# Performance work log

Measured on AMD Instinct MI355X. Metric: run time of the kernel, lower is better.

The kernel has to match this reference:

```python
import jax, jax.numpy as jnp
import numpy as np

C, PH, PW, H, W = 10, 7, 7, 34, 34
STRIDE = 8.0
S = 4  # sample_per_part


def setup_inputs() -> dict:
    key = jax.random.key(0)
    k1, k2, k3, k4, k5 = jax.random.split(key, 5)
    N = 30000
    ft = jax.random.normal(k1, (1, C * PH * PW, H, W), dtype=jnp.float32)
    x1 = jax.random.uniform(k2, (N,), dtype=jnp.float32) * 200.0
    y1 = jax.random.uniform(k3, (N,), dtype=jnp.float32) * 200.0
    bw = jax.random.uniform(k4, (N,), dtype=jnp.float32) * 70.0 + 2.0
    bh = jax.random.uniform(k5, (N,), dtype=jnp.float32) * 70.0 + 2.0
    rois = jnp.stack([jnp.zeros((N,), jnp.float32), x1, y1, x1 + bw, y1 + bh], axis=1)
    return {"ft_add_left_right": ft, "rois": rois}


def reference(ft_add_left_right, rois):
    ft = ft_add_left_right[0].reshape(C, PH, PW, H, W)
    roi_start_w = rois[:, 1] / STRIDE
    roi_start_h = rois[:, 2] / STRIDE
    roi_end_w = rois[:, 3] / STRIDE
    roi_end_h = rois[:, 4] / STRIDE
    # torch.threshold(x, 0.1, 0.1): x if x > 0.1 else 0.1
    roi_height = jnp.where(roi_end_h - roi_start_h > 0.1, roi_end_h - roi_start_h, 0.1)
    roi_width = jnp.where(roi_end_w - roi_start_w > 0.1, roi_end_w - roi_start_w, 0.1)
    bin_size_h = roi_height / PH
    bin_size_w = roi_width / PW
    sub_h = bin_size_h / S
    sub_w = bin_size_w / S

    gh, gw = jnp.meshgrid(jnp.arange(PH), jnp.arange(PW), indexing='ij')
    phs = gh.reshape(-1, 1)  # [49,1]
    pws = gw.reshape(-1, 1)  # [49,1]
    hstart = jnp.floor(roi_start_h + phs * bin_size_h)  # [49,N]
    wstart = jnp.floor(roi_start_w + pws * bin_size_w)  # [49,N]

    N = rois.shape[0]
    sum_ = jnp.zeros((C, PH * PW, N), jnp.float32)
    count = jnp.zeros((PH * PW, N), jnp.float32)

    for ih in range(S):
        for iw in range(S):
            w = wstart + (iw + 0.5) * sub_w  # [49,N]
            h = hstart + (ih + 0.5) * sub_h
            keep = (w > -1) & (w < W) & (h > -1) & (h < H)
            x1 = jnp.floor(w).astype(jnp.int32)
            x2 = jnp.ceil(w).astype(jnp.int32)
            y1 = jnp.floor(h).astype(jnp.int32)
            y2 = jnp.ceil(h).astype(jnp.int32)
            x1v = (x1 >= 0) & (x1 < W)
            x2v = (x2 >= 0) & (x2 < W)
            y1v = (y1 >= 0) & (y1 < H)
            y2v = (y2 >= 0) & (y2 < H)
            x1 = jnp.clip(x1, 0, W - 1)
            x2 = jnp.clip(x2, 0, W - 1)
            y1 = jnp.clip(y1, 0, H - 1)
            y2 = jnp.clip(y2, 0, H - 1)
            dist_x = w - x1
            dist_y = h - y1
            # gathers: result [C,49,N]
            v11 = ft[:, phs, pws, y1, x1]
            v12 = ft[:, phs, pws, y2, x1]
            v21 = ft[:, phs, pws, y1, x2]
            v22 = ft[:, phs, pws, y2, x2]
            # faithful to source: ALL four masks zero value11 only (source bug)
            bad11 = (~x1v & y1v) | (~x1v & y2v) | (~x2v & y1v) | (~x2v & y2v)
            v11 = jnp.where(bad11, 0.0, v11)
            value = ((1 - dist_x) * (1 - dist_y) * v11
                     + (1 - dist_x) * dist_y * v12
                     + dist_x * (1 - dist_y) * v21
                     + dist_x * dist_y * v22)
            sum_ = sum_ + jnp.where(keep, value, 0.0)
            count = count + keep.astype(jnp.float32)

    out = jnp.where(count > 0, sum_ / jnp.maximum(count, 1.0), sum_)
    return jnp.transpose(out, (2, 0, 1))  # [N, C, 49]
```

## Files before the change

kernel.cpp:

```cpp
#include <hip/hip_runtime.h>
#include <hip/hip_fp16.h>


#define NC 10
#define NBIN 49
#define FH 34
#define FW 34
#define PLANE (FH * FW)
#define NPIX (NBIN * PLANE)
#define RPB 16
#define TSTRIDE 491
#define NSIDE 14

__global__ __launch_bounds__(256) void prep_kernel(
    const float* __restrict__ ft, unsigned int* __restrict__ ws)
{
    const int p = blockIdx.x * 256 + threadIdx.x;
    if (p >= NPIX) return;
    unsigned int h2[5];
#pragma unroll
    for (int c = 0; c < 5; ++c) {
        const __half lo = __float2half_rn(ft[(2 * c)     * NPIX + p]);
        const __half hi = __float2half_rn(ft[(2 * c + 1) * NPIX + p]);
        const __half2 hh = __halves2half2(lo, hi);
        h2[c] = *(const unsigned int*)&hh;
    }
    *(uint4*)(ws + (size_t)p * 4) = make_uint4(h2[0], h2[1], h2[2], h2[3]);
    unsigned int* fb = ws + (size_t)NPIX * 4;
#pragma unroll
    for (int m = 0; m < 4; ++m)
        if (p >= m) fb[(size_t)m * NPIX + (p - m)] = h2[4];
}

__device__ __forceinline__ void fma2(float w, unsigned int u, float& s0, float& s1)
{
    const __half2 h = *(const __half2*)&u;
    s0 = fmaf(w, __half2float(__low2half(h)),  s0);
    s1 = fmaf(w, __half2float(__high2half(h)), s1);
}

__global__ __launch_bounds__(256) void main_kernel(
    const float* __restrict__ rois, const unsigned int* __restrict__ ftH,
    const float* __restrict__ ft, float* __restrict__ out, int N, int use_t)
{
    __shared__ float sides[NSIDE][RPB][8];
    __shared__ float tile[RPB][TSTRIDE];

    const int r = threadIdx.x & (RPB - 1);
    const int s = threadIdx.x >> 4;
    const int n = blockIdx.x * RPB + r;
    const bool valid = (n < N);

    float rsw = 0.f, rsh = 0.f, rew = 0.f, reh = 0.f;
    if (valid) {
        rsw = rois[n * 5 + 1] * 0.125f;
        rsh = rois[n * 5 + 2] * 0.125f;
        rew = rois[n * 5 + 3] * 0.125f;
        reh = rois[n * 5 + 4] * 0.125f;
    }
    float rheight = __fsub_rn(reh, rsh);
    if (!(rheight > 0.1f)) rheight = 0.1f;
    float rwidth = __fsub_rn(rew, rsw);
    if (!(rwidth > 0.1f)) rwidth = 0.1f;
    const float bsh   = __fdiv_rn(rheight, 7.0f);
    const float bsw   = __fdiv_rn(rwidth, 7.0f);
    const float sub_h = __fdiv_rn(bsh, 4.0f);
    const float sub_w = __fdiv_rn(bsw, 4.0f);

    if (s < NSIDE) {
        const bool isY = (s < 7);
        const int  k   = isY ? s : s - 7;
        const float st = isY ? rsh : rsw;
        const float bs = isY ? bsh : bsw;
        const float sb = isY ? sub_h : sub_w;
        const float start = floorf(__fadd_rn(st, __fmul_rn((float)k, bs)));

        float A[3] = {0.f, 0.f, 0.f}, B[3] = {0.f, 0.f, 0.f};
        float cnt = 0.f;
        int P0 = 0;
#pragma unroll
        for (int i = 0; i < 4; ++i) {
            const float h = __fadd_rn(start, __fmul_rn((float)i + 0.5f, sb));
            const bool ok = (h > -1.0f) && (h < 34.0f);
            const int p1 = (int)floorf(h);
            const int p2 = (int)ceilf(h);
            const bool v1 = (p1 >= 0) && (p1 < 34);
            const bool v2 = (p2 >= 0) && (p2 < 34);
            const int p1c = min(max(p1, 0), 33);
            const int p2c = min(max(p2, 0), 33);
            const float d = __fsub_rn(h, (float)p1c);
            if (i == 0) P0 = p1c;
            const int i1 = p1c - P0, i2 = p2c - P0;
            const float t1 = ok ? (1.0f - d) : 0.0f;
            const float t2 = ok ? d : 0.0f;
            const bool bsel = isY ? (v1 || v2) : ((!v1) || (!v2));
            const float tb = (ok && bsel) ? (1.0f - d) : 0.0f;
            cnt += ok ? 1.0f : 0.0f;
#pragma unroll
            for (int p = 0; p < 3; ++p) {
                A[p] += (i1 == p) ? t1 : 0.0f;
                A[p] += (i2 == p) ? t2 : 0.0f;
                B[p] += (i1 == p) ? tb : 0.0f;
            }
        }
        float* sp = &sides[s][r][0];
        sp[0] = A[0]; sp[1] = A[1]; sp[2] = A[2];
        sp[3] = B[0]; sp[4] = B[1]; sp[5] = B[2];
        sp[6] = cnt;  sp[7] = (float)P0;
    }
    __syncthreads();

#pragma unroll
    for (int j = 0; j < 4; ++j) {
        const int bin = j * RPB + s;
        if (valid && bin < NBIN) {
            const int ph = bin / 7;
            const int pw = bin - ph * 7;

            const float4 ya = *(const float4*)&sides[ph][r][0];
            const float4 yb = *(const float4*)&sides[ph][r][4];
            const float4 xa = *(const float4*)&sides[7 + pw][r][0];
            const float4 xb = *(const float4*)&sides[7 + pw][r][4];
            const float AY[3] = {ya.x, ya.y, ya.z};
            const float BY[3] = {ya.w, yb.x, yb.y};
            const float cntY  = yb.z;
            const int   Y0    = (int)yb.w;
            const float AX[3] = {xa.x, xa.y, xa.z};
            const float BX[3] = {xa.w, xb.x, xb.y};
            const float cntX  = xb.z;
            const int   X0    = (int)xb.w;

            const int binbase = bin * PLANE;
            const int rowo[3] = {binbase + Y0 * FW,
                                 binbase + min(Y0 + 1, FH - 1) * FW,
                                 binbase + min(Y0 + 2, FH - 1) * FW};
            const int colo[3] = {X0, min(X0 + 1, FW - 1), min(X0 + 2, FW - 1)};

            float wgt[9];
            int   off[9];
#pragma unroll
            for (int p = 0; p < 3; ++p)
#pragma unroll
                for (int q = 0; q < 3; ++q) {
                    const float w = AY[p] * AX[q] - BY[p] * BX[q];
                    wgt[3 * p + q] = w;
                    off[3 * p + q] = (w != 0.0f) ? (rowo[p] + colo[q]) : binbase;
                }

            float sum[NC];
#pragma unroll
            for (int c = 0; c < NC; ++c) sum[c] = 0.f;

            if (use_t) {
                const unsigned int* fB = ftH + (size_t)NPIX * 4;
                unsigned int rb[3][4];
#pragma unroll
                for (int p = 0; p < 3; ++p) {
                    const bool rnz = (wgt[3 * p]     != 0.0f) ||
                                     (wgt[3 * p + 1] != 0.0f) ||
                                     (wgt[3 * p + 2] != 0.0f);
                    const int fp = rnz ? (rowo[p] + X0) : binbase;
                    const int m  = fp & 3;
                    const int i0 = fp & ~3;
                    const uint4 V = *(const uint4*)(fB + (size_t)m * NPIX + i0);
                    rb[p][0] = V.x; rb[p][1] = V.y; rb[p][2] = V.z; rb[p][3] = V.w;
                }
#pragma unroll
                for (int k = 0; k < 9; ++k) {
                    const uint4 A = *(const uint4*)(ftH + (size_t)off[k] * 4);
                    const float w = wgt[k];
                    fma2(w, A.x, sum[0], sum[1]);
                    fma2(w, A.y, sum[2], sum[3]);
                    fma2(w, A.z, sum[4], sum[5]);
                    fma2(w, A.w, sum[6], sum[7]);
                }
                const int e = (FW - 1) - X0;
#pragma unroll
                for (int p = 0; p < 3; ++p) {
                    const unsigned int u0 = rb[p][0];
                    const unsigned int u1 = (e >= 1) ? rb[p][1] : rb[p][0];
                    const unsigned int u2 = (e >= 2) ? rb[p][2] : u1;
                    fma2(wgt[3 * p + 0], u0, sum[8], sum[9]);
                    fma2(wgt[3 * p + 1], u1, sum[8], sum[9]);
                    fma2(wgt[3 * p + 2], u2, sum[8], sum[9]);
                }
            } else {
#pragma unroll
                for (int k = 0; k < 9; ++k) {
                    const float w = wgt[k];
#pragma unroll
                    for (int c = 0; c < NC; ++c)
                        sum[c] = fmaf(w, ft[c * NPIX + off[k]], sum[c]);
                }
            }

            const float cnt = cntY * cntX;
            const float inv = (cnt > 0.0f) ? __fdiv_rn(1.0f, cnt) : 1.0f;
            float* tp = &tile[r][0];
#pragma unroll
            for (int c = 0; c < NC; ++c) tp[c * NBIN + bin] = sum[c] * inv;
        }
    }

    __syncthreads();

    const int n0 = blockIdx.x * RPB;
    for (int i = threadIdx.x; i < RPB * (NC * NBIN); i += 256) {
        const int row = i / (NC * NBIN);
        const int col = i - row * (NC * NBIN);
        const int n2 = n0 + row;
        if (n2 < N) out[(size_t)n2 * (NC * NBIN) + col] = tile[row][col];
    }
}

extern "C" void kernel_launch(void* const* d_in, const int* in_sizes, int n_in,
                              void* d_out, int out_size, void* d_ws, size_t ws_size,
                              hipStream_t stream) {
    const float* ft   = (const float*)d_in[0];
    const float* rois = (const float*)d_in[1];
    float* out        = (float*)d_out;
    const int N = in_sizes[1] / 5;

    const size_t need = (size_t)NPIX * 16 + (size_t)4 * NPIX * 4;
    const int use_t = (ws_size >= need) ? 1 : 0;
    unsigned int* ftH = (unsigned int*)d_ws;

    if (use_t) {
        prep_kernel<<<(NPIX + 255) / 256, 256, 0, stream>>>(ft, ftH);
    }
    main_kernel<<<(N + RPB - 1) / RPB, 256, 0, stream>>>(rois, ftH, ft, out, N, use_t);
}
```

Measured before the change: 109.5 us.

## Pack three-pixel row triplets of all channels into 64-byte workspace records

Reorganises the fp16 workspace so that each 64-byte record holds all 10 channels for three consecutive pixels, replicated at three alignment shifts. The main kernel then reads one record per bilinear row (four 16-byte loads) instead of nine scattered loads plus three extra loads for the last channel pair. Edge clamping is handled by folding the weights. It also adds a min-waves-per-EU hint (launch_bounds 256, 4). The cost is a larger prep write (three replicated copies of every pixel) and more registers per thread to hold the 45 loaded words.

```diff
diff --git a/kernel.cpp b/kernel.cpp
--- a/kernel.cpp
+++ b/kernel.cpp
@@ -8,28 +8,42 @@
 #define FW 34
 #define PLANE (FH * FW)
 #define NPIX (NBIN * PLANE)
+#define GPC 18882
 #define RPB 16
 #define TSTRIDE 491
 #define NSIDE 14
 
 __global__ __launch_bounds__(256) void prep_kernel(
-    const float* __restrict__ ft, unsigned int* __restrict__ ws)
+    const float* __restrict__ ft, unsigned int* __restrict__ ftR)
 {
     const int p = blockIdx.x * 256 + threadIdx.x;
-    if (p >= NPIX) return;
+    if (p >= NPIX + 2) return;
     unsigned int h2[5];
-#pragma unroll
-    for (int c = 0; c < 5; ++c) {
-        const __half lo = __float2half_rn(ft[(2 * c)     * NPIX + p]);
-        const __half hi = __float2half_rn(ft[(2 * c + 1) * NPIX + p]);
-        const __half2 hh = __halves2half2(lo, hi);
-        h2[c] = *(const unsigned int*)&hh;
-    }
-    *(uint4*)(ws + (size_t)p * 4) = make_uint4(h2[0], h2[1], h2[2], h2[3]);
-    unsigned int* fb = ws + (size_t)NPIX * 4;
-#pragma unroll
-    for (int m = 0; m < 4; ++m)
-        if (p >= m) fb[(size_t)m * NPIX + (p - m)] = h2[4];
+    if (p < NPIX) {
+#pragma unroll
+        for (int c = 0; c < 5; ++c) {
+            const __half lo = __float2half_rn(ft[(2 * c)     * NPIX + p]);
+            const __half hi = __float2half_rn(ft[(2 * c + 1) * NPIX + p]);
+            const __half2 hh = __halves2half2(lo, hi);
+            h2[c] = *(const unsigned int*)&hh;
+        }
+    } else {
+#pragma unroll
+        for (int c = 0; c < 5; ++c) h2[c] = 0u;
+    }
+#pragma unroll
+    for (int m = 0; m < 3; ++m) {
+        if (p >= m) {
+            const int t = p - m;
+            const int g = t / 3;
+            const int j = t - 3 * g;
+            if (g < GPC) {
+                unsigned int* d = ftR + ((size_t)m * GPC + g) * 16 + j * 5;
+#pragma unroll
+                for (int c = 0; c < 5; ++c) d[c] = h2[c];
+            }
+        }
+    }
 }
 
 __device__ __forceinline__ void fma2(float w, unsigned int u, float& s0, float& s1)
@@ -39,8 +53,8 @@
     s1 = fmaf(w, __half2float(__high2half(h)), s1);
 }
 
-__global__ __launch_bounds__(256) void main_kernel(
-    const float* __restrict__ rois, const unsigned int* __restrict__ ftH,
+__global__ __launch_bounds__(256, 4) void main_kernel(
+    const float* __restrict__ rois, const unsigned int* __restrict__ ftR,
     const float* __restrict__ ft, float* __restrict__ out, int N, int use_t)
 {
     __shared__ float sides[NSIDE][RPB][8];
@@ -134,57 +148,60 @@
             const int rowo[3] = {binbase + Y0 * FW,
                                  binbase + min(Y0 + 1, FH - 1) * FW,
                                  binbase + min(Y0 + 2, FH - 1) * FW};
-            const int colo[3] = {X0, min(X0 + 1, FW - 1), min(X0 + 2, FW - 1)};
 
             float wgt[9];
-            int   off[9];
 #pragma unroll
             for (int p = 0; p < 3; ++p)
 #pragma unroll
-                for (int q = 0; q < 3; ++q) {
-                    const float w = AY[p] * AX[q] - BY[p] * BX[q];
-                    wgt[3 * p + q] = w;
-                    off[3 * p + q] = (w != 0.0f) ? (rowo[p] + colo[q]) : binbase;
+                for (int q = 0; q < 3; ++q)
+                    wgt[3 * p + q] = AY[p] * AX[q] - BY[p] * BX[q];
+
+            float sum[NC];
+#pragma unroll
+            for (int c = 0; c < NC; ++c) sum[c] = 0.f;
+
+            if (use_t) {
+                const int e = (FW - 1) - X0;
+                unsigned int rv[3][15];
+                float ew[3][3];
+#pragma unroll
+                for (int p = 0; p < 3; ++p) {
+                    const float w0 = wgt[3 * p], w1 = wgt[3 * p + 1], w2 = wgt[3 * p + 2];
+                    const float s12 = w1 + w2;
+                    ew[p][0] = (e < 1) ? (w0 + s12) : w0;
+                    ew[p][1] = (e < 1) ? 0.f : ((e < 2) ? s12 : w1);
+                    ew[p][2] = (e < 2) ? 0.f : w2;
+                    const bool rnz = (w0 != 0.0f) || (w1 != 0.0f) || (w2 != 0.0f);
+                    const int fp = rnz ? (rowo[p] + X0) : binbase;
+                    const int g = fp / 3;
+                    const int m = fp - 3 * g;
+                    const unsigned int* lp = ftR + ((size_t)m * GPC + g) * 16;
+                    const uint4 a = *(const uint4*)lp;
+                    const uint4 b = *(const uint4*)(lp + 4);
+                    const uint4 c4 = *(const uint4*)(lp + 8);
+                    const uint4 d4 = *(const uint4*)(lp + 12);
+                    rv[p][0]  = a.x;  rv[p][1]  = a.y;  rv[p][2]  = a.z;  rv[p][3]  = a.w;
+                    rv[p][4]  = b.x;  rv[p][5]  = b.y;  rv[p][6]  = b.z;  rv[p][7]  = b.w;
+                    rv[p][8]  = c4.x; rv[p][9]  = c4.y; rv[p][10] = c4.z; rv[p][11] = c4.w;
+                    rv[p][12] = d4.x; rv[p][13] = d4.y; rv[p][14] = d4.z;
                 }
-
-            float sum[NC];
-#pragma unroll
-            for (int c = 0; c < NC; ++c) sum[c] = 0.f;
-
-            if (use_t) {
-                const unsigned int* fB = ftH + (size_t)NPIX * 4;
-                unsigned int rb[3][4];
-#pragma unroll
-                for (int p = 0; p < 3; ++p) {
-                    const bool rnz = (wgt[3 * p]     != 0.0f) ||
-                                     (wgt[3 * p + 1] != 0.0f) ||
-                                     (wgt[3 * p + 2] != 0.0f);
-                    const int fp = rnz ? (rowo[p] + X0) : binbase;
-                    const int m  = fp & 3;
-                    const int i0 = fp & ~3;
-                    const uint4 V = *(const uint4*)(fB + (size_t)m * NPIX + i0);
-                    rb[p][0] = V.x; rb[p][1] = V.y; rb[p][2] = V.z; rb[p][3] = V.w;
-                }
-#pragma unroll
-                for (int k = 0; k < 9; ++k) {
-                    const uint4 A = *(const uint4*)(ftH + (size_t)off[k] * 4);
-                    const float w = wgt[k];
-                    fma2(w, A.x, sum[0], sum[1]);
-                    fma2(w, A.y, sum[2], sum[3]);
-                    fma2(w, A.z, sum[4], sum[5]);
-                    fma2(w, A.w, sum[6], sum[7]);
-                }
-                const int e = (FW - 1) - X0;
-#pragma unroll
-                for (int p = 0; p < 3; ++p) {
-                    const unsigned int u0 = rb[p][0];
-                    const unsigned int u1 = (e >= 1) ? rb[p][1] : rb[p][0];
-                    const unsigned int u2 = (e >= 2) ? rb[p][2] : u1;
-                    fma2(wgt[3 * p + 0], u0, sum[8], sum[9]);
-                    fma2(wgt[3 * p + 1], u1, sum[8], sum[9]);
-                    fma2(wgt[3 * p + 2], u2, sum[8], sum[9]);
-                }
+#pragma unroll
+                for (int p = 0; p < 3; ++p)
+#pragma unroll
+                    for (int c = 0; c < 5; ++c) {
+                        fma2(ew[p][0], rv[p][c],      sum[2 * c], sum[2 * c + 1]);
+                        fma2(ew[p][1], rv[p][5 + c],  sum[2 * c], sum[2 * c + 1]);
+                        fma2(ew[p][2], rv[p][10 + c], sum[2 * c], sum[2 * c + 1]);
+                    }
             } else {
+                const int colo[3] = {X0, min(X0 + 1, FW - 1), min(X0 + 2, FW - 1)};
+                int off[9];
+#pragma unroll
+                for (int p = 0; p < 3; ++p)
+#pragma unroll
+                    for (int q = 0; q < 3; ++q)
+                        off[3 * p + q] = (wgt[3 * p + q] != 0.0f) ? (rowo[p] + colo[q])
+                                                                  : binbase;
 #pragma unroll
                 for (int k = 0; k < 9; ++k) {
                     const float w = wgt[k];
@@ -221,12 +238,12 @@
     float* out        = (float*)d_out;
     const int N = in_sizes[1] / 5;
 
-    const size_t need = (size_t)NPIX * 16 + (size_t)4 * NPIX * 4;
+    const size_t need = (size_t)3 * GPC * 64;
     const int use_t = (ws_size >= need) ? 1 : 0;
-    unsigned int* ftH = (unsigned int*)d_ws;
+    unsigned int* ftR = (unsigned int*)d_ws;
 
     if (use_t) {
-        prep_kernel<<<(NPIX + 255) / 256, 256, 0, stream>>>(ft, ftH);
-    }
-    main_kernel<<<(N + RPB - 1) / RPB, 256, 0, stream>>>(rois, ftH, ft, out, N, use_t);
-}
+        prep_kernel<<<(NPIX + 2 + 255) / 256, 256, 0, stream>>>(ft, ftR);
+    }
+    main_kernel<<<(N + RPB - 1) / RPB, 256, 0, stream>>>(rois, ftR, ft, out, N, use_t);
+}
```

Result: slower. 114.8 us (+4.9%).
